# Optimization experiments

Hardware: AMD Instinct MI355X
Metric: run time of the kernel (lower is better)

Reference implementation:

```python
import jax, jax.numpy as jnp
import numpy as np
from jax import lax

HEADS = 8
DIM_HEAD = 8
SCALE = DIM_HEAD ** (-0.5)
UP = 64  # nn.Upsample(scale_factor=64), nearest


def _conv_s8(x, w, b):
    # Conv2d(inner, inner, 11x11, stride 8, padding 2) + exact GELU
    y = lax.conv_general_dilated(x, w, window_strides=(8, 8),
                                 padding=((2, 2), (2, 2)),
                                 dimension_numbers=('NCHW', 'OIHW', 'NCHW'))
    return jax.nn.gelu(y + b[None, :, None, None], approximate=False)


def setup_inputs() -> dict:
    key = jax.random.key(0)
    ks = jax.random.split(key, 8)
    b, c, h, w = 2, 64, 48, 48
    inner = HEADS * DIM_HEAD  # 64
    f = jax.random.normal(ks[0], (b, c, h, w), jnp.float32)
    w_qkv = jax.random.normal(ks[1], (inner * 3, c, 1, 1), jnp.float32) * 0.05
    wq = jax.random.normal(ks[2], (inner, inner, 11, 11), jnp.float32) * 0.02
    bq = jax.random.normal(ks[3], (inner,), jnp.float32) * 0.02
    wk = jax.random.normal(ks[4], (inner, inner, 11, 11), jnp.float32) * 0.02
    bk = jax.random.normal(ks[5], (inner,), jnp.float32) * 0.02
    pos_h = jax.random.normal(ks[6], (DIM_HEAD, h), jnp.float32) * SCALE
    pos_w = jax.random.normal(ks[7], (DIM_HEAD, w), jnp.float32) * SCALE
    return {"f": f, "w_qkv": w_qkv, "wq": wq, "bq": bq, "wk": wk,
            "bk": bk, "pos_h": pos_h, "pos_w": pos_w}


def reference(f, w_qkv, wq, bq, wk, bk, pos_h, pos_w):
    b, c, h, w = f.shape
    inner = HEADS * DIM_HEAD
    # 1x1 conv to qkv
    qkv = jnp.einsum('oc,bchw->bohw', w_qkv[:, :, 0, 0], f)
    q, k, v = jnp.split(qkv, 3, axis=1)  # each [b, inner, h, w]
    # positional logits from pre-conv q
    q_full = q.reshape(b, HEADS, DIM_HEAD, h * w)
    emb = (pos_h[:, :, None] + pos_w[:, None, :]).reshape(DIM_HEAD, h * w)
    pos_logits = jnp.einsum('bhci,cj->bhij', q_full, emb)  # [b,H,hw,hw]
    # strided conv + gelu on q,k
    qd = _conv_s8(q, wq, bq)
    kd = _conv_s8(k, wk, bk)
    m = qd.shape[-1]  # downsampled side
    qd = qd.reshape(b, HEADS, DIM_HEAD, m * m) * SCALE
    kd = kd.reshape(b, HEADS, DIM_HEAD, m * m)
    vv = v.reshape(b, HEADS, DIM_HEAD, h * w)
    dots = jnp.einsum('bhci,bhcj->bhij', qd, kd)  # [b,H,m^2,m^2]
    # nearest upsample x64 on last two dims
    dots = jnp.repeat(jnp.repeat(dots, UP, axis=-2), UP, axis=-1)
    attn = jax.nn.softmax(dots + pos_logits, axis=-1)
    fmap = jnp.einsum('bhij,bhcj->bhci', attn, vv)
    return fmap.reshape(b, inner, h, w)
```

## Files before the change

### kernel.cpp

```cpp
#include <hip/hip_runtime.h>
#include <math.h>

#define HW 2304
#define O192 192
#define SCALE_F 0.35355339059327373f

typedef unsigned int u32;
typedef __attribute__((address_space(1))) const u32 gu32;
typedef __attribute__((address_space(3))) u32 lu32;
__device__ __forceinline__ void dma16(const void* g, void* l) {
  __builtin_amdgcn_global_load_lds((gu32*)g, (lu32*)l, 16, 0, 0);
}

__global__ __launch_bounds__(256) void qkv_kernel(
    const float* __restrict__ F, const float* __restrict__ W,
    float* __restrict__ QKV, float* __restrict__ V2) {
  __shared__ __align__(16) float sW[384];
  int blk = blockIdx.x;
  int idx0 = blk * 256;
  int r0 = idx0 / HW;
  int r1 = (idx0 + 255) / HW;
  int tid = threadIdx.x;
  if (tid < 192) {
    int g = tid >> 6, c = tid & 63;
    sW[tid]       = W[((r0 & 63) + g * 64) * 64 + c];
    sW[192 + tid] = W[((r1 & 63) + g * 64) * 64 + c];
  }
  __syncthreads();
  int idx = idx0 + tid;
  int p  = idx % HW;
  int r  = idx / HW;
  int o0 = r & 63;
  int b  = r >> 6;
  const float4* w4 = (const float4*)(sW + ((r == r0) ? 0 : 192));
  const float* f = F + (b * 64) * HW + p;
  float aq = 0.f, ak = 0.f, av = 0.f;
  #pragma unroll 4
  for (int c4 = 0; c4 < 16; c4++) {
    float4 wq = w4[c4];
    float4 wk = w4[16 + c4];
    float4 wv = w4[32 + c4];
    float f0 = f[(c4 * 4 + 0) * HW];
    float f1 = f[(c4 * 4 + 1) * HW];
    float f2 = f[(c4 * 4 + 2) * HW];
    float f3 = f[(c4 * 4 + 3) * HW];
    aq = fmaf(wq.x, f0, aq); ak = fmaf(wk.x, f0, ak); av = fmaf(wv.x, f0, av);
    aq = fmaf(wq.y, f1, aq); ak = fmaf(wk.y, f1, ak); av = fmaf(wv.y, f1, av);
    aq = fmaf(wq.z, f2, aq); ak = fmaf(wk.z, f2, ak); av = fmaf(wv.z, f2, av);
    aq = fmaf(wq.w, f3, aq); ak = fmaf(wk.w, f3, ak); av = fmaf(wv.w, f3, av);
  }
  float* qp = QKV + (b * HW + p) * O192;
  qp[o0]      = aq;
  qp[o0 + 64] = ak;
  V2[(((b << 3) + (o0 >> 3)) * HW + p) * 8 + (o0 & 7)] = av;
}

__global__ __launch_bounds__(256) void conv_kernel(
    const float* __restrict__ QKV, const float* __restrict__ Wq,
    const float* __restrict__ Bq, const float* __restrict__ Wk,
    const float* __restrict__ Bk, float* __restrict__ QD) {
  __shared__ float sW[7744];
  __shared__ float sRed[4 * 64 * 6];
  int blk = blockIdx.x;
  int xcd = blk & 7;
  int T = xcd >> 2, b = (xcd >> 1) & 1, s = xcd & 1;
  int idx = (blk >> 3) * 2 + s;
  int o  = idx / 6;
  int oy = idx % 6;
  const float* Wg = T ? Wk : Wq;
  for (int i = threadIdx.x; i < 7744; i += 256) sW[i] = Wg[o * 7744 + i];
  __syncthreads();
  int wv = threadIdx.x >> 6;
  int c  = threadIdx.x & 63;
  const float* base = QKV + b * (HW * O192) + T * 64 + c;
  float acc[6];
  #pragma unroll
  for (int ox = 0; ox < 6; ox++) acc[ox] = 0.f;
  for (int kyi = 0; kyi < 3; kyi++) {
    int ky = wv * 3 + kyi;
    if (ky > 10) break;
    int y = oy * 8 - 2 + ky;
    if ((unsigned)y < 48u) {
      float xrow[48];
      #pragma unroll
      for (int x = 0; x < 48; x++) xrow[x] = base[(y * 48 + x) * O192];
      #pragma unroll
      for (int kx = 0; kx < 11; kx++) {
        float wt = sW[c * 121 + ky * 11 + kx];
        #pragma unroll
        for (int ox = 0; ox < 6; ox++) {
          int x = ox * 8 - 2 + kx;
          if (x >= 0 && x < 48) acc[ox] = fmaf(xrow[x], wt, acc[ox]);
        }
      }
    }
  }
  #pragma unroll
  for (int ox = 0; ox < 6; ox++) sRed[(wv * 64 + c) * 6 + ox] = acc[ox];
  __syncthreads();
  if (threadIdx.x < 64) {
    int t = threadIdx.x;
    float r[6];
    #pragma unroll
    for (int ox = 0; ox < 6; ox++)
      r[ox] = sRed[t * 6 + ox] + sRed[(64 + t) * 6 + ox]
            + sRed[(128 + t) * 6 + ox] + sRed[(192 + t) * 6 + ox];
    #pragma unroll
    for (int off = 32; off; off >>= 1) {
      #pragma unroll
      for (int ox = 0; ox < 6; ox++) r[ox] += __shfl_down(r[ox], off, 64);
    }
    if (t == 0) {
      float bias = T ? Bk[o] : Bq[o];
      #pragma unroll
      for (int ox = 0; ox < 6; ox++) {
        float g = r[ox] + bias;
        float ge = 0.5f * g * (1.0f + erff(g * 0.70710678118654752f));
        QD[((T * 2 + b) * 64 + o) * 36 + oy * 6 + ox] = ge;
      }
    }
  }
}

__global__ __launch_bounds__(256) void dots_kernel(
    const float* __restrict__ QD, float* __restrict__ E) {
  int idx = blockIdx.x * 256 + threadIdx.x;
  if (idx >= 16 * 36 * 36) return;
  int J  = idx % 36;
  int I  = (idx / 36) % 36;
  int bh = idx / 1296;
  int b = bh >> 3, h = bh & 7;
  float acc = 0.f;
  #pragma unroll
  for (int c8 = 0; c8 < 8; c8++) {
    float qv = QD[((0 + b) * 64 + h * 8 + c8) * 36 + I];
    float kv = QD[((2 + b) * 64 + h * 8 + c8) * 36 + J];
    acc = fmaf(qv, kv, acc);
  }
  E[idx] = __expf(SCALE_F * acc);
}

#define OFF_V   0
#define OFF_EA  4608
#define OFF_PHT 7680
#define OFF_PWT 8064
#define OFF_E4  8448
#define OFF_U   8592
#define SBUF_N  13200

__global__ __launch_bounds__(512, 4) void attn_kernel(
    const float* __restrict__ QKV, const float* __restrict__ V2,
    const float* __restrict__ E, const float* __restrict__ PH,
    const float* __restrict__ PW, float* __restrict__ Pnum,
    float* __restrict__ PZ) {
  __shared__ __align__(16) float sB[SBUF_N];
  int blk = blockIdx.x;
  int bh = blk / 36;
  int rem = blk - bh * 36;
  int q = rem & 3, S = rem >> 2;
  int b = bh >> 3, h = bh & 7;
  int tid = threadIdx.x;
  int w = tid >> 6, lane = tid & 63;
  if (tid < 384) {
    sB[OFF_PHT + tid] = PH[(tid & 7) * 48 + (tid >> 3)];
    sB[OFF_PWT + tid] = PW[(tid & 7) * 48 + (tid >> 3)];
  }
  if (tid < 144) {
    int J = tid >> 2, k = tid & 3;
    sB[OFF_E4 + tid] = E[bh * 1296 + (S * 4 + k) * 36 + J];
  }
  {
    int row = tid >> 1, half = tid & 1;
    *(float4*)(sB + OFF_U + tid * 4) =
      *(const float4*)(QKV + (b * HW + S * 256 + row) * O192 + h * 8 + half * 4);
  }
  {
    const char* src = (const char*)(V2 + (size_t)bh * (HW * 8) + q * 4608);
    for (int m = w; m < 18; m += 8)
      dma16(src + m * 1024 + lane * 16, (char*)(sB + OFF_V) + m * 1024);
  }
  __syncthreads();
  #pragma unroll
  for (int m = 0; m < 6; m++) {
    int flat = tid + m * 512;
    int jyL = flat >> 8, rl = flat & 255;
    int ln = rl >> 2, kk = rl & 3;
    const float* qp = sB + OFF_U + (kk * 64 + ln) * 8;
    const float* pp = sB + OFF_PHT + (q * 12 + jyL) * 8;
    float d = qp[0]*pp[0]+qp[1]*pp[1]+qp[2]*pp[2]+qp[3]*pp[3]
            + qp[4]*pp[4]+qp[5]*pp[5]+qp[6]*pp[6]+qp[7]*pp[7];
    sB[OFF_EA + flat] = __expf(d);
  }
  float eB[4][6];
  #pragma unroll
  for (int k = 0; k < 4; k++) {
    const float* qp = sB + OFF_U + (k * 64 + lane) * 8;
    #pragma unroll
    for (int i = 0; i < 6; i++) {
      const float* pp = sB + OFF_PWT + (w * 6 + i) * 8;
      float d = qp[0]*pp[0]+qp[1]*pp[1]+qp[2]*pp[2]+qp[3]*pp[3]
              + qp[4]*pp[4]+qp[5]*pp[5]+qp[6]*pp[6]+qp[7]*pp[7];
      eB[k][i] = __expf(d);
    }
  }
  __syncthreads();
  float acc[4][9];
  #pragma unroll
  for (int k = 0; k < 4; k++)
    #pragma unroll
    for (int c = 0; c < 9; c++) acc[k][c] = 0.f;
  const float4* sV4 = (const float4*)(sB + OFF_V);
  for (int jyL = 0; jyL < 12; jyL++) {
    float4 eAk = *(const float4*)(sB + OFF_EA + jyL * 256 + lane * 4);
    int cb = (q * 12 + jyL) * 48 + w * 6;
    int J0 = cb >> 6, J1 = (cb + 5) >> 6;
    int ib = 64 - (cb & 63);
    float4 e0 = *(const float4*)(sB + OFF_E4 + J0 * 4);
    float4 e1 = *(const float4*)(sB + OFF_E4 + J1 * 4);
    float a0[4] = {eAk.x*e0.x, eAk.y*e0.y, eAk.z*e0.z, eAk.w*e0.w};
    float a1[4] = {eAk.x*e1.x, eAk.y*e1.y, eAk.z*e1.z, eAk.w*e1.w};
    #pragma unroll
    for (int i = 0; i < 6; i++) {
      float4 vlo = sV4[(jyL * 48 + w * 6 + i) * 2];
      float4 vhi = sV4[(jyL * 48 + w * 6 + i) * 2 + 1];
      bool sel = (i < ib);
      #pragma unroll
      for (int k = 0; k < 4; k++) {
        float wgt = (sel ? a0[k] : a1[k]) * eB[k][i];
        acc[k][0] = fmaf(wgt, vlo.x, acc[k][0]);
        acc[k][1] = fmaf(wgt, vlo.y, acc[k][1]);
        acc[k][2] = fmaf(wgt, vlo.z, acc[k][2]);
        acc[k][3] = fmaf(wgt, vlo.w, acc[k][3]);
        acc[k][4] = fmaf(wgt, vhi.x, acc[k][4]);
        acc[k][5] = fmaf(wgt, vhi.y, acc[k][5]);
        acc[k][6] = fmaf(wgt, vhi.z, acc[k][6]);
        acc[k][7] = fmaf(wgt, vhi.w, acc[k][7]);
        acc[k][8] += wgt;
      }
    }
  }
  float* sU = sB + OFF_U;
  #pragma unroll
  for (int k = 0; k < 4; k++) {
    #pragma unroll
    for (int c = 0; c < 9; c++) sU[(w * 64 + lane) * 9 + c] = acc[k][c];
    __syncthreads();
    {
      int c = tid >> 6, r = tid & 63;
      float num = 0.f;
      #pragma unroll
      for (int ww = 0; ww < 8; ww++) num += sU[(ww * 64 + r) * 9 + c];
      Pnum[((q * 16 + bh) * 8 + c) * HW + S * 256 + k * 64 + r] = num;
      if (tid < 64) {
        float z = 0.f;
        #pragma unroll
        for (int ww = 0; ww < 8; ww++) z += sU[(ww * 64 + tid) * 9 + 8];
        PZ[(q * 16 + bh) * HW + S * 256 + k * 64 + tid] = z;
      }
    }
    __syncthreads();
  }
}

__global__ __launch_bounds__(256) void combine_kernel(
    const float* __restrict__ Pnum, const float* __restrict__ PZ,
    float* __restrict__ out) {
  int t = blockIdx.x * 256 + threadIdx.x;
  int row = t % HW;
  int rc = t / HW;
  int c = rc & 7, bh = rc >> 3;
  float num = 0.f, z = 0.f;
  #pragma unroll
  for (int q = 0; q < 4; q++) {
    num += Pnum[((q * 16 + bh) * 8 + c) * HW + row];
    z   += PZ[(q * 16 + bh) * HW + row];
  }
  int b = bh >> 3, h = bh & 7;
  out[(b * 64 + h * 8 + c) * HW + row] = num / z;
}

extern "C" void kernel_launch(void* const* d_in, const int* in_sizes, int n_in,
                              void* d_out, int out_size, void* d_ws, size_t ws_size,
                              hipStream_t stream) {
  const float* F    = (const float*)d_in[0];
  const float* Wqkv = (const float*)d_in[1];
  const float* Wq   = (const float*)d_in[2];
  const float* Bq   = (const float*)d_in[3];
  const float* Wk   = (const float*)d_in[4];
  const float* Bk   = (const float*)d_in[5];
  const float* PH   = (const float*)d_in[6];
  const float* PW   = (const float*)d_in[7];
  float* out = (float*)d_out;

  float* ws   = (float*)d_ws;
  float* QKV  = ws;
  float* V2   = QKV + 2 * HW * O192;
  float* QD   = V2 + 2 * 8 * HW * 8;
  float* E    = QD + 2 * 2 * 64 * 36;
  float* Pnum = E + 16 * 36 * 36;
  float* PZ   = Pnum + 4 * 16 * 8 * HW;

  qkv_kernel    <<<1152, 256, 0, stream>>>(F, Wqkv, QKV, V2);
  conv_kernel   <<<1536, 256, 0, stream>>>(QKV, Wq, Bq, Wk, Bk, QD);
  dots_kernel   <<<81,   256, 0, stream>>>(QD, E);
  attn_kernel   <<<576,  512, 0, stream>>>(QKV, V2, E, PH, PW, Pnum, PZ);
  combine_kernel<<<1152, 256, 0, stream>>>(Pnum, PZ, out);
}
```

Measured before the change: 141.8 us.

## Fuse dots kernel into attention and split channels across half-waves

Removes the separate dots kernel: each attention block computes its own 36x4 exp(q·k) slice straight from QD, dropping one launch and the E round-trip through memory. The attention inner loop is also reorganised so each half-wave takes 4 of the 8 value channels across 8 query rows instead of all 8 channels for 4 rows. This halves the V loads per thread and cuts LDS use, at the cost of duplicating the positional exp work (eB) and the Z accumulation in both halves. The reduction epilogue is restructured to match the new layout, with Z summed from both halves and halved.

```diff
diff --git a/kernel.cpp b/kernel.cpp
--- a/kernel.cpp
+++ b/kernel.cpp
@@ -122,35 +122,17 @@
   }
 }
 
-__global__ __launch_bounds__(256) void dots_kernel(
-    const float* __restrict__ QD, float* __restrict__ E) {
-  int idx = blockIdx.x * 256 + threadIdx.x;
-  if (idx >= 16 * 36 * 36) return;
-  int J  = idx % 36;
-  int I  = (idx / 36) % 36;
-  int bh = idx / 1296;
-  int b = bh >> 3, h = bh & 7;
-  float acc = 0.f;
-  #pragma unroll
-  for (int c8 = 0; c8 < 8; c8++) {
-    float qv = QD[((0 + b) * 64 + h * 8 + c8) * 36 + I];
-    float kv = QD[((2 + b) * 64 + h * 8 + c8) * 36 + J];
-    acc = fmaf(qv, kv, acc);
-  }
-  E[idx] = __expf(SCALE_F * acc);
-}
-
 #define OFF_V   0
 #define OFF_EA  4608
 #define OFF_PHT 7680
 #define OFF_PWT 8064
 #define OFF_E4  8448
 #define OFF_U   8592
-#define SBUF_N  13200
+#define SBUF_N  11152
 
 __global__ __launch_bounds__(512, 4) void attn_kernel(
     const float* __restrict__ QKV, const float* __restrict__ V2,
-    const float* __restrict__ E, const float* __restrict__ PH,
+    const float* __restrict__ QD, const float* __restrict__ PH,
     const float* __restrict__ PW, float* __restrict__ Pnum,
     float* __restrict__ PZ) {
   __shared__ __align__(16) float sB[SBUF_N];
@@ -161,13 +143,19 @@
   int b = bh >> 3, h = bh & 7;
   int tid = threadIdx.x;
   int w = tid >> 6, lane = tid & 63;
+  int l32 = lane & 31, chalf = lane >> 5;
   if (tid < 384) {
     sB[OFF_PHT + tid] = PH[(tid & 7) * 48 + (tid >> 3)];
     sB[OFF_PWT + tid] = PW[(tid & 7) * 48 + (tid >> 3)];
   }
   if (tid < 144) {
-    int J = tid >> 2, k = tid & 3;
-    sB[OFF_E4 + tid] = E[bh * 1296 + (S * 4 + k) * 36 + J];
+    int J = tid >> 2, k4 = tid & 3;
+    const float* qd = QD + ((0 + b) * 64 + h * 8) * 36 + (S * 4 + k4);
+    const float* kd = QD + ((2 + b) * 64 + h * 8) * 36 + J;
+    float acc = 0.f;
+    #pragma unroll
+    for (int c8 = 0; c8 < 8; c8++) acc = fmaf(qd[c8 * 36], kd[c8 * 36], acc);
+    sB[OFF_E4 + J * 4 + k4] = __expf(SCALE_F * acc);
   }
   {
     int row = tid >> 1, half = tid & 1;
@@ -183,82 +171,97 @@
   #pragma unroll
   for (int m = 0; m < 6; m++) {
     int flat = tid + m * 512;
-    int jyL = flat >> 8, rl = flat & 255;
-    int ln = rl >> 2, kk = rl & 3;
-    const float* qp = sB + OFF_U + (kk * 64 + ln) * 8;
+    int jyL = flat >> 8, row = flat & 255;
+    const float* qp = sB + OFF_U + row * 8;
     const float* pp = sB + OFF_PHT + (q * 12 + jyL) * 8;
     float d = qp[0]*pp[0]+qp[1]*pp[1]+qp[2]*pp[2]+qp[3]*pp[3]
             + qp[4]*pp[4]+qp[5]*pp[5]+qp[6]*pp[6]+qp[7]*pp[7];
-    sB[OFF_EA + flat] = __expf(d);
-  }
-  float eB[4][6];
-  #pragma unroll
-  for (int k = 0; k < 4; k++) {
-    const float* qp = sB + OFF_U + (k * 64 + lane) * 8;
+    sB[OFF_EA + jyL * 256 + (row & 31) * 8 + (row >> 5)] = __expf(d);
+  }
+  float pw[6][8];
+  #pragma unroll
+  for (int i = 0; i < 6; i++) {
+    float4 a = *(const float4*)(sB + OFF_PWT + (w * 6 + i) * 8);
+    float4 c = *(const float4*)(sB + OFF_PWT + (w * 6 + i) * 8 + 4);
+    pw[i][0]=a.x; pw[i][1]=a.y; pw[i][2]=a.z; pw[i][3]=a.w;
+    pw[i][4]=c.x; pw[i][5]=c.y; pw[i][6]=c.z; pw[i][7]=c.w;
+  }
+  float eB[8][6];
+  #pragma unroll
+  for (int k8 = 0; k8 < 8; k8++) {
+    const float* qp = sB + OFF_U + (k8 * 32 + l32) * 8;
+    float4 qa = *(const float4*)qp;
+    float4 qb = *(const float4*)(qp + 4);
     #pragma unroll
     for (int i = 0; i < 6; i++) {
-      const float* pp = sB + OFF_PWT + (w * 6 + i) * 8;
-      float d = qp[0]*pp[0]+qp[1]*pp[1]+qp[2]*pp[2]+qp[3]*pp[3]
-              + qp[4]*pp[4]+qp[5]*pp[5]+qp[6]*pp[6]+qp[7]*pp[7];
-      eB[k][i] = __expf(d);
-    }
-  }
-  __syncthreads();
-  float acc[4][9];
-  #pragma unroll
-  for (int k = 0; k < 4; k++)
-    #pragma unroll
-    for (int c = 0; c < 9; c++) acc[k][c] = 0.f;
+      float d = qa.x*pw[i][0]+qa.y*pw[i][1]+qa.z*pw[i][2]+qa.w*pw[i][3]
+              + qb.x*pw[i][4]+qb.y*pw[i][5]+qb.z*pw[i][6]+qb.w*pw[i][7];
+      eB[k8][i] = __expf(d);
+    }
+  }
+  float accv[8][4], zz[8];
+  #pragma unroll
+  for (int k8 = 0; k8 < 8; k8++) {
+    zz[k8] = 0.f;
+    #pragma unroll
+    for (int c = 0; c < 4; c++) accv[k8][c] = 0.f;
+  }
+  __syncthreads();
   const float4* sV4 = (const float4*)(sB + OFF_V);
   for (int jyL = 0; jyL < 12; jyL++) {
-    float4 eAk = *(const float4*)(sB + OFF_EA + jyL * 256 + lane * 4);
+    float4 ea0 = *(const float4*)(sB + OFF_EA + jyL * 256 + l32 * 8);
+    float4 ea1 = *(const float4*)(sB + OFF_EA + jyL * 256 + l32 * 8 + 4);
     int cb = (q * 12 + jyL) * 48 + w * 6;
     int J0 = cb >> 6, J1 = (cb + 5) >> 6;
     int ib = 64 - (cb & 63);
     float4 e0 = *(const float4*)(sB + OFF_E4 + J0 * 4);
     float4 e1 = *(const float4*)(sB + OFF_E4 + J1 * 4);
-    float a0[4] = {eAk.x*e0.x, eAk.y*e0.y, eAk.z*e0.z, eAk.w*e0.w};
-    float a1[4] = {eAk.x*e1.x, eAk.y*e1.y, eAk.z*e1.z, eAk.w*e1.w};
+    float a0[8], a1[8];
+    a0[0]=ea0.x*e0.x; a0[1]=ea0.y*e0.x; a0[2]=ea0.z*e0.y; a0[3]=ea0.w*e0.y;
+    a0[4]=ea1.x*e0.z; a0[5]=ea1.y*e0.z; a0[6]=ea1.z*e0.w; a0[7]=ea1.w*e0.w;
+    a1[0]=ea0.x*e1.x; a1[1]=ea0.y*e1.x; a1[2]=ea0.z*e1.y; a1[3]=ea0.w*e1.y;
+    a1[4]=ea1.x*e1.z; a1[5]=ea1.y*e1.z; a1[6]=ea1.z*e1.w; a1[7]=ea1.w*e1.w;
     #pragma unroll
     for (int i = 0; i < 6; i++) {
-      float4 vlo = sV4[(jyL * 48 + w * 6 + i) * 2];
-      float4 vhi = sV4[(jyL * 48 + w * 6 + i) * 2 + 1];
-      bool sel = (i < ib);
-      #pragma unroll
-      for (int k = 0; k < 4; k++) {
-        float wgt = (sel ? a0[k] : a1[k]) * eB[k][i];
-        acc[k][0] = fmaf(wgt, vlo.x, acc[k][0]);
-        acc[k][1] = fmaf(wgt, vlo.y, acc[k][1]);
-        acc[k][2] = fmaf(wgt, vlo.z, acc[k][2]);
-        acc[k][3] = fmaf(wgt, vlo.w, acc[k][3]);
-        acc[k][4] = fmaf(wgt, vhi.x, acc[k][4]);
-        acc[k][5] = fmaf(wgt, vhi.y, acc[k][5]);
-        acc[k][6] = fmaf(wgt, vhi.z, acc[k][6]);
-        acc[k][7] = fmaf(wgt, vhi.w, acc[k][7]);
-        acc[k][8] += wgt;
+      float4 v = sV4[(jyL * 48 + w * 6 + i) * 2 + chalf];
+      bool s0 = (i < ib);
+      #pragma unroll
+      for (int k8 = 0; k8 < 8; k8++) {
+        float wgt = (s0 ? a0[k8] : a1[k8]) * eB[k8][i];
+        accv[k8][0] = fmaf(wgt, v.x, accv[k8][0]);
+        accv[k8][1] = fmaf(wgt, v.y, accv[k8][1]);
+        accv[k8][2] = fmaf(wgt, v.z, accv[k8][2]);
+        accv[k8][3] = fmaf(wgt, v.w, accv[k8][3]);
+        zz[k8] += wgt;
       }
     }
   }
   float* sU = sB + OFF_U;
   #pragma unroll
-  for (int k = 0; k < 4; k++) {
-    #pragma unroll
-    for (int c = 0; c < 9; c++) sU[(w * 64 + lane) * 9 + c] = acc[k][c];
+  for (int k8 = 0; k8 < 8; k8++) {
     __syncthreads();
     {
-      int c = tid >> 6, r = tid & 63;
+      float* rp = sU + (w * 64 + lane) * 5;
+      rp[0] = accv[k8][0]; rp[1] = accv[k8][1];
+      rp[2] = accv[k8][2]; rp[3] = accv[k8][3];
+      rp[4] = zz[k8];
+    }
+    __syncthreads();
+    if (tid < 256) {
+      int row32 = tid & 31, c = tid >> 5;
+      int ln = row32 + (c >> 2) * 32;
       float num = 0.f;
       #pragma unroll
-      for (int ww = 0; ww < 8; ww++) num += sU[(ww * 64 + r) * 9 + c];
-      Pnum[((q * 16 + bh) * 8 + c) * HW + S * 256 + k * 64 + r] = num;
-      if (tid < 64) {
-        float z = 0.f;
-        #pragma unroll
-        for (int ww = 0; ww < 8; ww++) z += sU[(ww * 64 + tid) * 9 + 8];
-        PZ[(q * 16 + bh) * HW + S * 256 + k * 64 + tid] = z;
-      }
-    }
-    __syncthreads();
+      for (int ww = 0; ww < 8; ww++) num += sU[(ww * 64 + ln) * 5 + (c & 3)];
+      Pnum[((q * 16 + bh) * 8 + c) * HW + S * 256 + k8 * 32 + row32] = num;
+    } else if (tid < 288) {
+      int row32 = tid & 31;
+      float z = 0.f;
+      #pragma unroll
+      for (int ww = 0; ww < 8; ww++)
+        z += sU[(ww * 64 + row32) * 5 + 4] + sU[(ww * 64 + 32 + row32) * 5 + 4];
+      PZ[(q * 16 + bh) * HW + S * 256 + k8 * 32 + row32] = z * 0.5f;
+    }
   }
 }
 
@@ -296,13 +299,11 @@
   float* QKV  = ws;
   float* V2   = QKV + 2 * HW * O192;
   float* QD   = V2 + 2 * 8 * HW * 8;
-  float* E    = QD + 2 * 2 * 64 * 36;
-  float* Pnum = E + 16 * 36 * 36;
+  float* Pnum = QD + 2 * 2 * 64 * 36;
   float* PZ   = Pnum + 4 * 16 * 8 * HW;
 
   qkv_kernel    <<<1152, 256, 0, stream>>>(F, Wqkv, QKV, V2);
   conv_kernel   <<<1536, 256, 0, stream>>>(QKV, Wq, Bq, Wk, Bk, QD);
-  dots_kernel   <<<81,   256, 0, stream>>>(QD, E);
-  attn_kernel   <<<576,  512, 0, stream>>>(QKV, V2, E, PH, PW, Pnum, PZ);
+  attn_kernel   <<<576,  512, 0, stream>>>(QKV, V2, QD, PH, PW, Pnum, PZ);
   combine_kernel<<<1152, 256, 0, stream>>>(Pnum, PZ, out);
 }
```

Result: slower. 159.5 us (+12.5%).
